# Performance work log

Hardware: AMD Instinct MI355X
Metric: run time of the kernel (lower is better)

Reference implementation:

```python
import jax, jax.numpy as jnp
import numpy as np

TEMP = 8.0      # config.router_temp
TOP_K = 2       # config.moe_top_k
EPS = 1e-8
LN_EPS = 1e-5


def _layer_norm_noaffine(x):
    # nn.LayerNorm(input_dim, elementwise_affine=False)
    mu = jnp.mean(x, axis=-1, keepdims=True)
    var = jnp.var(x, axis=-1, keepdims=True)
    return (x - mu) / jnp.sqrt(var + LN_EPS)


def _unit_norm(x):
    # x / x.norm(dim=-1).clamp(min=EPS)
    n = jnp.linalg.norm(x, axis=-1, keepdims=True)
    return x / jnp.maximum(n, EPS)


def setup_inputs() -> dict:
    key = jax.random.key(0)
    k1, k2 = jax.random.split(key)
    x = jax.random.normal(k1, (4, 4096, 2048), dtype=jnp.float32)
    prototypes = jax.random.normal(k2, (64, 2048), dtype=jnp.float32)
    return {"x": x, "prototypes": prototypes}


def reference(x, prototypes):
    # input_norm_fn = 'norm_d', proto_norm_fn = 'unit'
    xn = _layer_norm_noaffine(x)          # [b, s, d]
    pn = _unit_norm(prototypes)           # [e, d]
    logits = jnp.einsum('bsd,ed->bse', xn, pn) / TEMP   # [b, s, e]
    probs = jax.nn.softmax(logits, axis=-1)
    top_w, top_i = jax.lax.top_k(probs, TOP_K)          # [b, s, k]
    top_w = top_w / jnp.sum(top_w, axis=-1, keepdims=True)
    return top_w, top_i
```

## Files before the change

### kernel.cpp

```cpp
#include <hip/hip_runtime.h>
#include <math.h>

typedef __attribute__((ext_vector_type(8))) short short8;
typedef __attribute__((ext_vector_type(4))) float f32x4;

constexpr int kD  = 2048;
constexpr int kE  = 64;
constexpr int kM  = 32;
constexpr int kBK = 128;
constexpr int kIt = kD / kBK;
constexpr int kTS  = 3136;
constexpr int kCS2 = 2 * kTS;
constexpr int kBuf = 4 * kCS2;

constexpr int kPlaneU = 4 * 64 * 512;
__device__ unsigned short g_B[3 * kPlaneU];

__device__ __forceinline__ void split3(float v, unsigned& h, unsigned& m, unsigned& l) {
  unsigned u = __float_as_uint(v);
  h = u & 0xFFFF0000u;
  float r1 = v - __uint_as_float(h);
  m = __float_as_uint(r1) & 0xFFFF0000u;
  float r2 = r1 - __uint_as_float(m);
  l = __float_as_uint(r2);
}

__device__ __forceinline__ void pack2(float e0, float e1,
                                      unsigned& dh, unsigned& dm, unsigned& dl) {
  unsigned h0, m0, l0, h1, m1, l1;
  split3(e0, h0, m0, l0);
  split3(e1, h1, m1, l1);
  dh = (h0 >> 16) | h1;
  dm = (m0 >> 16) | m1;
  dl = (l0 >> 16) | (l1 & 0xFFFF0000u);
}

__global__ __launch_bounds__(256) void proto_prep(const float* __restrict__ p,
                                                  float* __restrict__ ws) {
  const int e = blockIdx.x, t = threadIdx.x;
  const float* row = p + (size_t)e * kD;
  float4 v0 = *(const float4*)(row + 8 * t);
  float4 v1 = *(const float4*)(row + 8 * t + 4);

  unsigned dh[4], dm[4], dl[4];
  pack2(v0.x, v0.y, dh[0], dm[0], dl[0]);
  pack2(v0.z, v0.w, dh[1], dm[1], dl[1]);
  pack2(v1.x, v1.y, dh[2], dm[2], dl[2]);
  pack2(v1.z, v1.w, dh[3], dm[3], dl[3]);
  const int gc = t >> 2, o = t & 3;
  size_t base = (size_t)((e >> 4) * 64 + gc) * 512 + (16 * o + (e & 15)) * 8;
  *(uint4*)&g_B[base]               = make_uint4(dh[0], dh[1], dh[2], dh[3]);
  *(uint4*)&g_B[kPlaneU + base]     = make_uint4(dm[0], dm[1], dm[2], dm[3]);
  *(uint4*)&g_B[2 * kPlaneU + base] = make_uint4(dl[0], dl[1], dl[2], dl[3]);

  float s = (v0.x + v0.y) + (v0.z + v0.w) + (v1.x + v1.y) + (v1.z + v1.w);
  float q = v0.x*v0.x + v0.y*v0.y + v0.z*v0.z + v0.w*v0.w
          + v1.x*v1.x + v1.y*v1.y + v1.z*v1.z + v1.w*v1.w;
  #pragma unroll
  for (int off = 32; off >= 1; off >>= 1) {
    s += __shfl_xor(s, off, 64);
    q += __shfl_xor(q, off, 64);
  }
  __shared__ float as[4], aq[4];
  if ((t & 63) == 0) { as[t >> 6] = s; aq[t >> 6] = q; }
  __syncthreads();
  if (t == 0) {
    float S = (as[0] + as[1]) + (as[2] + as[3]);
    float Q = (aq[0] + aq[1]) + (aq[2] + aq[3]);
    ws[e]      = S;
    ws[kE + e] = 1.f / fmaxf(sqrtf(Q), 1e-8f);
  }
}

__global__ __launch_bounds__(256, 2) void router_main(
    const float* __restrict__ x, const float* __restrict__ ws,
    float* __restrict__ out_w, float* __restrict__ out_i) {
  __shared__ __align__(16) unsigned char sA[2 * kBuf];
  __shared__ float sLogit[kM * 68];
  __shared__ float sStats[kM][2];

  const int t    = threadIdx.x;
  const int w    = t >> 6;
  const int L    = t & 63;
  const int ln15 = L & 15;
  const int q    = L >> 4;
  const int tok0 = blockIdx.x * kM;
  const float* xg = x + (size_t)tok0 * kD;

  const int mB = t >> 5;
  const int kc = (t & 31) * 4;
  const int c_s = kc >> 5;
  const int o_s = (kc >> 3) & 3;
  const int j_s = kc & 7;
  const int wcol = (16 * o_s) * 48 + o_s * 16 + j_s * 2;

  f32x4 acc0 = (f32x4){0.f, 0.f, 0.f, 0.f};
  f32x4 acc1 = (f32x4){0.f, 0.f, 0.f, 0.f};
  float sx[4]  = {0.f, 0.f, 0.f, 0.f};
  float sxx[4] = {0.f, 0.f, 0.f, 0.f};

  auto stage = [&](const float4 v, float& sxr, float& sxxr, int m, unsigned char* wb) {
    unsigned dh0, dm0, dl0, dh1, dm1, dl1;
    pack2(v.x, v.y, dh0, dm0, dl0);
    pack2(v.z, v.w, dh1, dm1, dl1);
    sxr += (v.x + v.y) + (v.z + v.w);
    sxxr = fmaf(v.x, v.x, fmaf(v.y, v.y, fmaf(v.z, v.z, fmaf(v.w, v.w, sxxr))));
    unsigned char* dst = wb + c_s * kCS2 + (m >> 4) * kTS + (m & 15) * 48 + wcol;
    *(uint2*)(dst)      = make_uint2(dh0, dh1);
    *(uint2*)(dst + 16) = make_uint2(dm0, dm1);
    *(uint2*)(dst + 32) = make_uint2(dl0, dl1);
  };

  float4 pfA[4], pfB[4];
  #pragma unroll
  for (int jj = 0; jj < 4; ++jj)
    pfA[jj] = *(const float4*)(xg + (size_t)(mB + 8 * jj) * kD + kc);
  #pragma unroll
  for (int jj = 0; jj < 4; ++jj)
    stage(pfA[jj], sx[jj], sxx[jj], mB + 8 * jj, sA);
  #pragma unroll
  for (int jj = 0; jj < 4; ++jj)
    pfA[jj] = *(const float4*)(xg + (size_t)(mB + 8 * jj) * kD + kBK + kc);

  short8 Bh, Bm, Bl;
  {
    const size_t bo = (size_t)(w * 64) * 512 + L * 8;
    Bh = *(const short8*)&g_B[bo];
    Bm = *(const short8*)&g_B[kPlaneU + bo];
    Bl = *(const short8*)&g_B[2 * kPlaneU + bo];
  }
  __syncthreads();

  const int aoff = L * 48 + (L >> 4) * 16;

  for (int it = 0; it < kIt; ++it) {
    unsigned char* rbase = sA + (it & 1) * kBuf;
    unsigned char* wbase = sA + ((it & 1) ^ 1) * kBuf;

    if (it + 2 < kIt) {
      #pragma unroll
      for (int jj = 0; jj < 4; ++jj)
        pfB[jj] = *(const float4*)(xg + (size_t)(mB + 8 * jj) * kD + (it + 2) * kBK + kc);
    }

    const unsigned char* ra = rbase + aoff;
    short8 Ah0 = *(const short8*)(ra);
    short8 Am0 = *(const short8*)(ra + 16);
    short8 Al0 = *(const short8*)(ra + 32);
    short8 Ah1 = *(const short8*)(ra + kTS);
    short8 Am1 = *(const short8*)(ra + kTS + 16);
    short8 Al1 = *(const short8*)(ra + kTS + 32);

    const bool do_stage = (it + 1 < kIt);

    #pragma unroll
    for (int c = 0; c < 4; ++c) {
      const int ngc = (it * 4 + c + 1) & 63;
      const size_t nbo = (size_t)(w * 64 + ngc) * 512 + L * 8;
      short8 nBh = *(const short8*)&g_B[nbo];
      short8 nBm = *(const short8*)&g_B[kPlaneU + nbo];
      short8 nBl = *(const short8*)&g_B[2 * kPlaneU + nbo];

      short8 nAh0 = Ah0, nAm0 = Am0, nAl0 = Al0;
      short8 nAh1 = Ah1, nAm1 = Am1, nAl1 = Al1;
      if (c < 3) {
        const unsigned char* rn = rbase + (c + 1) * kCS2 + aoff;
        nAh0 = *(const short8*)(rn);
        nAm0 = *(const short8*)(rn + 16);
        nAl0 = *(const short8*)(rn + 32);
        nAh1 = *(const short8*)(rn + kTS);
        nAm1 = *(const short8*)(rn + kTS + 16);
        nAl1 = *(const short8*)(rn + kTS + 32);
      }

      acc0 = __builtin_amdgcn_mfma_f32_16x16x32_bf16(Ah0, Bh, acc0, 0, 0, 0);
      acc1 = __builtin_amdgcn_mfma_f32_16x16x32_bf16(Ah1, Bh, acc1, 0, 0, 0);
      acc0 = __builtin_amdgcn_mfma_f32_16x16x32_bf16(Ah0, Bm, acc0, 0, 0, 0);
      acc1 = __builtin_amdgcn_mfma_f32_16x16x32_bf16(Ah1, Bm, acc1, 0, 0, 0);
      acc0 = __builtin_amdgcn_mfma_f32_16x16x32_bf16(Am0, Bh, acc0, 0, 0, 0);
      acc1 = __builtin_amdgcn_mfma_f32_16x16x32_bf16(Am1, Bh, acc1, 0, 0, 0);
      acc0 = __builtin_amdgcn_mfma_f32_16x16x32_bf16(Am0, Bm, acc0, 0, 0, 0);
      acc1 = __builtin_amdgcn_mfma_f32_16x16x32_bf16(Am1, Bm, acc1, 0, 0, 0);
      acc0 = __builtin_amdgcn_mfma_f32_16x16x32_bf16(Ah0, Bl, acc0, 0, 0, 0);
      acc1 = __builtin_amdgcn_mfma_f32_16x16x32_bf16(Ah1, Bl, acc1, 0, 0, 0);
      acc0 = __builtin_amdgcn_mfma_f32_16x16x32_bf16(Al0, Bh, acc0, 0, 0, 0);
      acc1 = __builtin_amdgcn_mfma_f32_16x16x32_bf16(Al1, Bh, acc1, 0, 0, 0);

      if (do_stage)
        stage(pfA[c], sx[c], sxx[c], mB + 8 * c, wbase);

      Bh = nBh; Bm = nBm; Bl = nBl;
      Ah0 = nAh0; Am0 = nAm0; Al0 = nAl0;
      Ah1 = nAh1; Am1 = nAm1; Al1 = nAl1;
    }

    __syncthreads();
    if (it + 2 < kIt) {
      #pragma unroll
      for (int jj = 0; jj < 4; ++jj) pfA[jj] = pfB[jj];
    }
  }

  #pragma unroll
  for (int jj = 0; jj < 4; ++jj) {
    float a = sx[jj], b = sxx[jj];
    #pragma unroll
    for (int off = 16; off >= 1; off >>= 1) {
      a += __shfl_xor(a, off, 64);
      b += __shfl_xor(b, off, 64);
    }
    if ((L & 31) == 0) {
      int m = mB + 8 * jj;
      sStats[m][0] = a;
      sStats[m][1] = b;
    }
  }

  #pragma unroll
  for (int i = 0; i < 4; ++i) {
    sLogit[(q * 4 + i) * 68 + w * 16 + ln15]      = acc0[i];
    sLogit[(16 + q * 4 + i) * 68 + w * 16 + ln15] = acc1[i];
  }
  __syncthreads();

  const float Se  = ws[L];
  const float inv = ws[kE + L];
  #pragma unroll
  for (int tl = 0; tl < 8; ++tl) {
    int tk = w * 8 + tl;
    float mu   = sStats[tk][0] * (1.f / kD);
    float var  = sStats[tk][1] * (1.f / kD) - mu * mu;
    float rstd = rsqrtf(var + 1e-5f);
    float logit = (sLogit[tk * 68 + L] - mu * Se) * rstd * inv * 0.125f;

    float v1 = logit; int i1 = L;
    #pragma unroll
    for (int off = 32; off >= 1; off >>= 1) {
      float ov = __shfl_xor(v1, off, 64);
      int   oi = __shfl_xor(i1, off, 64);
      if (ov > v1 || (ov == v1 && oi < i1)) { v1 = ov; i1 = oi; }
    }
    float ml = (L == i1) ? -3.402823466e38f : logit;
    float v2 = ml; int i2 = L;
    #pragma unroll
    for (int off = 32; off >= 1; off >>= 1) {
      float ov = __shfl_xor(v2, off, 64);
      int   oi = __shfl_xor(i2, off, 64);
      if (ov > v2 || (ov == v2 && oi < i2)) { v2 = ov; i2 = oi; }
    }
    if (L == 0) {
      int tg = tok0 + tk;
      float er = expf(v2 - v1);
      float r  = 1.f / (1.f + er);
      out_w[2 * tg]     = r;
      out_w[2 * tg + 1] = er * r;
      out_i[2 * tg]     = (float)i1;
      out_i[2 * tg + 1] = (float)i2;
    }
  }
}

extern "C" void kernel_launch(void* const* d_in, const int* in_sizes, int n_in,
                              void* d_out, int out_size, void* d_ws, size_t ws_size,
                              hipStream_t stream) {
  const float* x = (const float*)d_in[0];
  const float* p = (const float*)d_in[1];
  float* ws = (float*)d_ws;
  const int T = in_sizes[0] / kD;
  float* out_w = (float*)d_out;
  float* out_i = (float*)d_out + (size_t)T * 2;

  proto_prep<<<kE, 256, 0, stream>>>(p, ws);
  router_main<<<T / kM, 256, 0, stream>>>(x, ws, out_w, out_i);
}
```

Measured before the change: 209.8 us.

## Switch to 32x32x16 MFMA with K-split across waves and new LDS layout

Replaces the 16x16x32 bf16 MFMA tiling, where each wave owned 16 experts over the full K, with 32x32x16 MFMAs. Each wave now owns 32 experts and half of each K chunk, and the two K halves are reduced through shared memory at the end. The shared-memory layout for the split-bf16 x tiles and the global prototype plane layout are rearranged to match the new operand shapes. B loads are prefetched one step ahead, and s_setprio is added around the MFMA bursts. The intent is fewer MFMA issues and better operand reuse, at the cost of a larger sLogit buffer, an extra cross-wave reduction and higher register pressure from 16-wide accumulators.

```diff
diff --git a/kernel.cpp b/kernel.cpp
--- a/kernel.cpp
+++ b/kernel.cpp
@@ -1,19 +1,21 @@
 #include <hip/hip_runtime.h>
 #include <math.h>
 
-typedef __attribute__((ext_vector_type(8))) short short8;
-typedef __attribute__((ext_vector_type(4))) float f32x4;
+typedef __attribute__((ext_vector_type(8)))  short short8;
+typedef __attribute__((ext_vector_type(16))) float f32x16;
 
 constexpr int kD  = 2048;
 constexpr int kE  = 64;
 constexpr int kM  = 32;
 constexpr int kBK = 128;
 constexpr int kIt = kD / kBK;
-constexpr int kTS  = 3136;
-constexpr int kCS2 = 2 * kTS;
-constexpr int kBuf = 4 * kCS2;
-
-constexpr int kPlaneU = 4 * 64 * 512;
+
+constexpr int kOS  = 544;
+constexpr int kPS  = 4 * kOS;
+constexpr int kGS  = 3 * kPS + 16;
+constexpr int kBuf = 4 * kGS;
+
+constexpr int kPlaneU = 2 * 64 * 2 * 64 * 8;
 __device__ unsigned short g_B[3 * kPlaneU];
 
 __device__ __forceinline__ void split3(float v, unsigned& h, unsigned& m, unsigned& l) {
@@ -47,8 +49,11 @@
   pack2(v0.z, v0.w, dh[1], dm[1], dl[1]);
   pack2(v1.x, v1.y, dh[2], dm[2], dl[2]);
   pack2(v1.z, v1.w, dh[3], dm[3], dl[3]);
-  const int gc = t >> 2, o = t & 3;
-  size_t base = (size_t)((e >> 4) * 64 + gc) * 512 + (16 * o + (e & 15)) * 8;
+  const int gc = t >> 2;
+  const int kh = (t >> 1) & 1;
+  const int lb = t & 1;
+  size_t base = ((((size_t)(e >> 5) * 64 + gc) * 2 + kh) * 64
+                 + ((e & 31) | (lb << 5))) * 8;
   *(uint4*)&g_B[base]               = make_uint4(dh[0], dh[1], dh[2], dh[3]);
   *(uint4*)&g_B[kPlaneU + base]     = make_uint4(dm[0], dm[1], dm[2], dm[3]);
   *(uint4*)&g_B[2 * kPlaneU + base] = make_uint4(dl[0], dl[1], dl[2], dl[3]);
@@ -76,26 +81,27 @@
     const float* __restrict__ x, const float* __restrict__ ws,
     float* __restrict__ out_w, float* __restrict__ out_i) {
   __shared__ __align__(16) unsigned char sA[2 * kBuf];
-  __shared__ float sLogit[kM * 68];
+  __shared__ float sLogit[2 * kM * 68];
   __shared__ float sStats[kM][2];
 
   const int t    = threadIdx.x;
   const int w    = t >> 6;
   const int L    = t & 63;
-  const int ln15 = L & 15;
-  const int q    = L >> 4;
+  const int eg   = w & 1;
+  const int kp   = w >> 1;
   const int tok0 = blockIdx.x * kM;
   const float* xg = x + (size_t)tok0 * kD;
 
   const int mB = t >> 5;
   const int kc = (t & 31) * 4;
-  const int c_s = kc >> 5;
-  const int o_s = (kc >> 3) & 3;
-  const int j_s = kc & 7;
-  const int wcol = (16 * o_s) * 48 + o_s * 16 + j_s * 2;
-
-  f32x4 acc0 = (f32x4){0.f, 0.f, 0.f, 0.f};
-  f32x4 acc1 = (f32x4){0.f, 0.f, 0.f, 0.f};
+  const int gcS = kc >> 5;
+  const int oS  = (kc >> 3) & 3;
+  const int jS  = kc & 7;
+  const int wOff = gcS * kGS + oS * kOS + jS * 2;
+
+  f32x16 accA = {0.f}, accB = {0.f};
+  #pragma unroll
+  for (int i = 0; i < 16; ++i) { accA[i] = 0.f; accB[i] = 0.f; }
   float sx[4]  = {0.f, 0.f, 0.f, 0.f};
   float sxx[4] = {0.f, 0.f, 0.f, 0.f};
 
@@ -105,10 +111,14 @@
     pack2(v.z, v.w, dh1, dm1, dl1);
     sxr += (v.x + v.y) + (v.z + v.w);
     sxxr = fmaf(v.x, v.x, fmaf(v.y, v.y, fmaf(v.z, v.z, fmaf(v.w, v.w, sxxr))));
-    unsigned char* dst = wb + c_s * kCS2 + (m >> 4) * kTS + (m & 15) * 48 + wcol;
-    *(uint2*)(dst)      = make_uint2(dh0, dh1);
-    *(uint2*)(dst + 16) = make_uint2(dm0, dm1);
-    *(uint2*)(dst + 32) = make_uint2(dl0, dl1);
+    unsigned char* dst = wb + wOff + m * 16;
+    *(uint2*)(dst)           = make_uint2(dh0, dh1);
+    *(uint2*)(dst + kPS)     = make_uint2(dm0, dm1);
+    *(uint2*)(dst + 2 * kPS) = make_uint2(dl0, dl1);
+  };
+
+  auto bIdx = [&](int g, int kh) -> size_t {
+    return ((((size_t)eg * 64 + g) * 2 + kh) * 64 + L) * 8;
   };
 
   float4 pfA[4], pfB[4];
@@ -121,21 +131,28 @@
   #pragma unroll
   for (int jj = 0; jj < 4; ++jj)
     pfA[jj] = *(const float4*)(xg + (size_t)(mB + 8 * jj) * kD + kBK + kc);
-
-  short8 Bh, Bm, Bl;
+  #pragma unroll
+  for (int jj = 0; jj < 4; ++jj) pfB[jj] = pfA[jj];
+
+  short8 BcH0, BcM0, BcL0, BcH1, BcM1, BcL1;
   {
-    const size_t bo = (size_t)(w * 64) * 512 + L * 8;
-    Bh = *(const short8*)&g_B[bo];
-    Bm = *(const short8*)&g_B[kPlaneU + bo];
-    Bl = *(const short8*)&g_B[2 * kPlaneU + bo];
+    size_t b0 = bIdx(kp, 0), b1 = bIdx(kp, 1);
+    BcH0 = *(const short8*)&g_B[b0];
+    BcM0 = *(const short8*)&g_B[kPlaneU + b0];
+    BcL0 = *(const short8*)&g_B[2 * kPlaneU + b0];
+    BcH1 = *(const short8*)&g_B[b1];
+    BcM1 = *(const short8*)&g_B[kPlaneU + b1];
+    BcL1 = *(const short8*)&g_B[2 * kPlaneU + b1];
   }
   __syncthreads();
 
-  const int aoff = L * 48 + (L >> 4) * 16;
+  const int aRow = (L & 31) * 16;
+  const int aOct = (L >> 5) * kOS;
 
   for (int it = 0; it < kIt; ++it) {
-    unsigned char* rbase = sA + (it & 1) * kBuf;
-    unsigned char* wbase = sA + ((it & 1) ^ 1) * kBuf;
+    unsigned char* rb = sA + (it & 1) * kBuf;
+    unsigned char* wb = sA + ((it & 1) ^ 1) * kBuf;
+    const bool do_stage = (it + 1 < kIt);
 
     if (it + 2 < kIt) {
       #pragma unroll
@@ -143,56 +160,88 @@
         pfB[jj] = *(const float4*)(xg + (size_t)(mB + 8 * jj) * kD + (it + 2) * kBK + kc);
     }
 
-    const unsigned char* ra = rbase + aoff;
-    short8 Ah0 = *(const short8*)(ra);
-    short8 Am0 = *(const short8*)(ra + 16);
-    short8 Al0 = *(const short8*)(ra + 32);
-    short8 Ah1 = *(const short8*)(ra + kTS);
-    short8 Am1 = *(const short8*)(ra + kTS + 16);
-    short8 Al1 = *(const short8*)(ra + kTS + 32);
-
-    const bool do_stage = (it + 1 < kIt);
-
-    #pragma unroll
-    for (int c = 0; c < 4; ++c) {
-      const int ngc = (it * 4 + c + 1) & 63;
-      const size_t nbo = (size_t)(w * 64 + ngc) * 512 + L * 8;
-      short8 nBh = *(const short8*)&g_B[nbo];
-      short8 nBm = *(const short8*)&g_B[kPlaneU + nbo];
-      short8 nBl = *(const short8*)&g_B[2 * kPlaneU + nbo];
-
-      short8 nAh0 = Ah0, nAm0 = Am0, nAl0 = Al0;
-      short8 nAh1 = Ah1, nAm1 = Am1, nAl1 = Al1;
-      if (c < 3) {
-        const unsigned char* rn = rbase + (c + 1) * kCS2 + aoff;
-        nAh0 = *(const short8*)(rn);
-        nAm0 = *(const short8*)(rn + 16);
-        nAl0 = *(const short8*)(rn + 32);
-        nAh1 = *(const short8*)(rn + kTS);
-        nAm1 = *(const short8*)(rn + kTS + 16);
-        nAl1 = *(const short8*)(rn + kTS + 32);
-      }
-
-      acc0 = __builtin_amdgcn_mfma_f32_16x16x32_bf16(Ah0, Bh, acc0, 0, 0, 0);
-      acc1 = __builtin_amdgcn_mfma_f32_16x16x32_bf16(Ah1, Bh, acc1, 0, 0, 0);
-      acc0 = __builtin_amdgcn_mfma_f32_16x16x32_bf16(Ah0, Bm, acc0, 0, 0, 0);
-      acc1 = __builtin_amdgcn_mfma_f32_16x16x32_bf16(Ah1, Bm, acc1, 0, 0, 0);
-      acc0 = __builtin_amdgcn_mfma_f32_16x16x32_bf16(Am0, Bh, acc0, 0, 0, 0);
-      acc1 = __builtin_amdgcn_mfma_f32_16x16x32_bf16(Am1, Bh, acc1, 0, 0, 0);
-      acc0 = __builtin_amdgcn_mfma_f32_16x16x32_bf16(Am0, Bm, acc0, 0, 0, 0);
-      acc1 = __builtin_amdgcn_mfma_f32_16x16x32_bf16(Am1, Bm, acc1, 0, 0, 0);
-      acc0 = __builtin_amdgcn_mfma_f32_16x16x32_bf16(Ah0, Bl, acc0, 0, 0, 0);
-      acc1 = __builtin_amdgcn_mfma_f32_16x16x32_bf16(Ah1, Bl, acc1, 0, 0, 0);
-      acc0 = __builtin_amdgcn_mfma_f32_16x16x32_bf16(Al0, Bh, acc0, 0, 0, 0);
-      acc1 = __builtin_amdgcn_mfma_f32_16x16x32_bf16(Al1, Bh, acc1, 0, 0, 0);
-
-      if (do_stage)
-        stage(pfA[c], sx[c], sxx[c], mB + 8 * c, wbase);
-
-      Bh = nBh; Bm = nBm; Bl = nBl;
-      Ah0 = nAh0; Am0 = nAm0; Al0 = nAl0;
-      Ah1 = nAh1; Am1 = nAm1; Al1 = nAl1;
-    }
+    const unsigned char* ra = rb + kp * kGS + aOct + aRow;
+    short8 AH0 = *(const short8*)(ra);
+    short8 AM0 = *(const short8*)(ra + kPS);
+    short8 AL0 = *(const short8*)(ra + 2 * kPS);
+    short8 AH1 = *(const short8*)(ra + 2 * kOS);
+    short8 AM1 = *(const short8*)(ra + 2 * kOS + kPS);
+    short8 AL1 = *(const short8*)(ra + 2 * kOS + 2 * kPS);
+
+    short8 BnH0, BnM0, BnL0, BnH1, BnM1, BnL1;
+    {
+      const int g1 = it * 4 + 2 + kp;
+      size_t b0 = bIdx(g1, 0), b1 = bIdx(g1, 1);
+      BnH0 = *(const short8*)&g_B[b0];
+      BnM0 = *(const short8*)&g_B[kPlaneU + b0];
+      BnL0 = *(const short8*)&g_B[2 * kPlaneU + b0];
+      BnH1 = *(const short8*)&g_B[b1];
+      BnM1 = *(const short8*)&g_B[kPlaneU + b1];
+      BnL1 = *(const short8*)&g_B[2 * kPlaneU + b1];
+    }
+
+    if (do_stage) {
+      stage(pfA[0], sx[0], sxx[0], mB,     wb);
+      stage(pfA[1], sx[1], sxx[1], mB + 8, wb);
+    }
+
+    __builtin_amdgcn_s_setprio(1);
+    accA = __builtin_amdgcn_mfma_f32_32x32x16_bf16(AH0, BcH0, accA, 0, 0, 0);
+    accB = __builtin_amdgcn_mfma_f32_32x32x16_bf16(AH1, BcH1, accB, 0, 0, 0);
+    accA = __builtin_amdgcn_mfma_f32_32x32x16_bf16(AH0, BcM0, accA, 0, 0, 0);
+    accB = __builtin_amdgcn_mfma_f32_32x32x16_bf16(AH1, BcM1, accB, 0, 0, 0);
+    accA = __builtin_amdgcn_mfma_f32_32x32x16_bf16(AM0, BcH0, accA, 0, 0, 0);
+    accB = __builtin_amdgcn_mfma_f32_32x32x16_bf16(AM1, BcH1, accB, 0, 0, 0);
+    accA = __builtin_amdgcn_mfma_f32_32x32x16_bf16(AM0, BcM0, accA, 0, 0, 0);
+    accB = __builtin_amdgcn_mfma_f32_32x32x16_bf16(AM1, BcM1, accB, 0, 0, 0);
+    accA = __builtin_amdgcn_mfma_f32_32x32x16_bf16(AH0, BcL0, accA, 0, 0, 0);
+    accB = __builtin_amdgcn_mfma_f32_32x32x16_bf16(AH1, BcL1, accB, 0, 0, 0);
+    accA = __builtin_amdgcn_mfma_f32_32x32x16_bf16(AL0, BcH0, accA, 0, 0, 0);
+    accB = __builtin_amdgcn_mfma_f32_32x32x16_bf16(AL1, BcH1, accB, 0, 0, 0);
+    __builtin_amdgcn_s_setprio(0);
+
+    const unsigned char* rc = rb + (2 + kp) * kGS + aOct + aRow;
+    AH0 = *(const short8*)(rc);
+    AM0 = *(const short8*)(rc + kPS);
+    AL0 = *(const short8*)(rc + 2 * kPS);
+    AH1 = *(const short8*)(rc + 2 * kOS);
+    AM1 = *(const short8*)(rc + 2 * kOS + kPS);
+    AL1 = *(const short8*)(rc + 2 * kOS + 2 * kPS);
+
+    short8 BfH0, BfM0, BfL0, BfH1, BfM1, BfL1;
+    {
+      const int gN = ((it + 1) * 4 + kp) & 63;
+      size_t b0 = bIdx(gN, 0), b1 = bIdx(gN, 1);
+      BfH0 = *(const short8*)&g_B[b0];
+      BfM0 = *(const short8*)&g_B[kPlaneU + b0];
+      BfL0 = *(const short8*)&g_B[2 * kPlaneU + b0];
+      BfH1 = *(const short8*)&g_B[b1];
+      BfM1 = *(const short8*)&g_B[kPlaneU + b1];
+      BfL1 = *(const short8*)&g_B[2 * kPlaneU + b1];
+    }
+
+    if (do_stage) {
+      stage(pfA[2], sx[2], sxx[2], mB + 16, wb);
+      stage(pfA[3], sx[3], sxx[3], mB + 24, wb);
+    }
+
+    __builtin_amdgcn_s_setprio(1);
+    accA = __builtin_amdgcn_mfma_f32_32x32x16_bf16(AH0, BnH0, accA, 0, 0, 0);
+    accB = __builtin_amdgcn_mfma_f32_32x32x16_bf16(AH1, BnH1, accB, 0, 0, 0);
+    accA = __builtin_amdgcn_mfma_f32_32x32x16_bf16(AH0, BnM0, accA, 0, 0, 0);
+    accB = __builtin_amdgcn_mfma_f32_32x32x16_bf16(AH1, BnM1, accB, 0, 0, 0);
+    accA = __builtin_amdgcn_mfma_f32_32x32x16_bf16(AM0, BnH0, accA, 0, 0, 0);
+    accB = __builtin_amdgcn_mfma_f32_32x32x16_bf16(AM1, BnH1, accB, 0, 0, 0);
+    accA = __builtin_amdgcn_mfma_f32_32x32x16_bf16(AM0, BnM0, accA, 0, 0, 0);
+    accB = __builtin_amdgcn_mfma_f32_32x32x16_bf16(AM1, BnM1, accB, 0, 0, 0);
+    accA = __builtin_amdgcn_mfma_f32_32x32x16_bf16(AH0, BnL0, accA, 0, 0, 0);
+    accB = __builtin_amdgcn_mfma_f32_32x32x16_bf16(AH1, BnL1, accB, 0, 0, 0);
+    accA = __builtin_amdgcn_mfma_f32_32x32x16_bf16(AL0, BnH0, accA, 0, 0, 0);
+    accB = __builtin_amdgcn_mfma_f32_32x32x16_bf16(AL1, BnH1, accB, 0, 0, 0);
+    __builtin_amdgcn_s_setprio(0);
+
+    BcH0 = BfH0; BcM0 = BfM0; BcL0 = BfL0;
+    BcH1 = BfH1; BcM1 = BfM1; BcL1 = BfL1;
 
     __syncthreads();
     if (it + 2 < kIt) {
@@ -217,9 +266,9 @@
   }
 
   #pragma unroll
-  for (int i = 0; i < 4; ++i) {
-    sLogit[(q * 4 + i) * 68 + w * 16 + ln15]      = acc0[i];
-    sLogit[(16 + q * 4 + i) * 68 + w * 16 + ln15] = acc1[i];
+  for (int i = 0; i < 16; ++i) {
+    int row = (i & 3) + 8 * (i >> 2) + 4 * (L >> 5);
+    sLogit[(kp * kM + row) * 68 + eg * 32 + (L & 31)] = accA[i] + accB[i];
   }
   __syncthreads();
 
@@ -231,7 +280,8 @@
     float mu   = sStats[tk][0] * (1.f / kD);
     float var  = sStats[tk][1] * (1.f / kD) - mu * mu;
     float rstd = rsqrtf(var + 1e-5f);
-    float logit = (sLogit[tk * 68 + L] - mu * Se) * rstd * inv * 0.125f;
+    float dot  = sLogit[tk * 68 + L] + sLogit[(kM + tk) * 68 + L];
+    float logit = (dot - mu * Se) * rstd * inv * 0.125f;
 
     float v1 = logit; int i1 = L;
     #pragma unroll
```

Measured after the change: 207.1 us. Within noise of the previous version (-1.3%).
